# Performance work log

Hardware: AMD Instinct MI355X
Metric: run time of the kernel (lower is better)

Reference implementation:

```python
import jax, jax.numpy as jnp
import numpy as np

# dims: batch, seq, d_model, heads, n_buckets, n_hashes, d_ff
B, S, D, H, NB, R, DFF = 2, 4096, 1024, 16, 64, 4, 4096
DH = D // H          # head dim
C = S // NB          # attention chunk length after bucket sort
NCH = S // C         # number of chunks


def layernorm(x, g, b):
    m = x.mean(-1, keepdims=True)
    v = ((x - m) ** 2).mean(-1, keepdims=True)
    return (x - m) / jnp.sqrt(v + 1e-5) * g + b


def lsh_attention(x, Wqk, Wv, Wo, rot):
    Bx, Sx, _ = x.shape
    # shared QK projection (Reformer-style), separate V
    qk = (x @ Wqk).reshape(Bx, Sx, H, DH).transpose(0, 2, 1, 3)  # [B,H,S,dh]
    v = (x @ Wv).reshape(Bx, Sx, H, DH).transpose(0, 2, 1, 3)
    # random-rotation LSH: rot [dh, R, NB//2]
    rotated = jnp.einsum('bhsd,drk->rbhsk', qk, rot)
    buckets = jnp.argmax(jnp.concatenate([rotated, -rotated], -1), -1)  # [R,B,H,S]
    scale = DH ** -0.5
    pos = jnp.arange(Sx)

    def one_round(b_r):  # b_r: [B,H,S] bucket ids for one hash round
        order = jnp.argsort(b_r * Sx + pos, axis=-1)   # stable sort by bucket
        inv = jnp.argsort(order, axis=-1)
        sqk = jnp.take_along_axis(qk, order[..., None], 2)
        sv = jnp.take_along_axis(v, order[..., None], 2)
        sb = jnp.take_along_axis(b_r, order, -1)
        q_c = sqk.reshape(Bx, H, NCH, C, DH)
        # keys are L2-normalized shared qk
        k_c = (sqk / (jnp.linalg.norm(sqk, axis=-1, keepdims=True) + 1e-6)).reshape(Bx, H, NCH, C, DH)
        v_c = sv.reshape(Bx, H, NCH, C, DH)
        ext = lambda t: jnp.concatenate([t, jnp.roll(t, 1, axis=2)], axis=3)  # look back 1 chunk
        k_e, v_e = ext(k_c), ext(v_c)
        b_c = sb.reshape(Bx, H, NCH, C)
        b_e = jnp.concatenate([b_c, jnp.roll(b_c, 1, axis=2)], 3)
        p_c = order.reshape(Bx, H, NCH, C)
        p_e = jnp.concatenate([p_c, jnp.roll(p_c, 1, axis=2)], 3)
        s = jnp.einsum('bhnqd,bhnkd->bhnqk', q_c, k_e) * scale  # [B,H,nch,C,2C]
        s = jnp.where(b_c[..., :, None] == b_e[..., None, :], s, -1e9)   # only same bucket
        s = jnp.where(p_c[..., :, None] == p_e[..., None, :], -1e5, s)   # discourage self
        l = jax.scipy.special.logsumexp(s, -1)
        o = jnp.einsum('bhnqk,bhnkd->bhnqd', jax.nn.softmax(s, -1), v_e)
        o = o.reshape(Bx, H, Sx, DH)
        l = l.reshape(Bx, H, Sx)
        return jnp.take_along_axis(o, inv[..., None], 2), jnp.take_along_axis(l, inv, -1)

    o_all, l_all = jax.vmap(one_round)(buckets)        # [R,B,H,S,dh], [R,B,H,S]
    w = jax.nn.softmax(l_all, axis=0)[..., None]       # weight rounds by logsumexp
    out = (o_all * w).sum(0).transpose(0, 2, 1, 3).reshape(Bx, Sx, D)
    return out @ Wo


def feedforward(x, W1, b1, W2, b2):
    # chunked FF in the original only tiles the sequence dim; math is identical
    return jax.nn.relu(x @ W1 + b1) @ W2 + b2


def setup_inputs() -> dict:
    key = jax.random.key(0)
    ks = jax.random.split(key, 10)
    n = jax.random.normal
    return {
        'x1': n(ks[0], (B, S, D), jnp.float32),
        'x2': n(ks[1], (B, S, D), jnp.float32),
        'Wqk': n(ks[2], (D, D), jnp.float32) * (D ** -0.5),
        'Wv': n(ks[3], (D, D), jnp.float32) * (D ** -0.5),
        'Wo': n(ks[4], (D, D), jnp.float32) * (D ** -0.5),
        'ln1_g': jnp.ones(D, jnp.float32), 'ln1_b': jnp.zeros(D, jnp.float32),
        'W1': n(ks[5], (D, DFF), jnp.float32) * (D ** -0.5), 'bf1': jnp.zeros(DFF, jnp.float32),
        'W2': n(ks[6], (DFF, D), jnp.float32) * (DFF ** -0.5), 'bf2': jnp.zeros(D, jnp.float32),
        'ln2_g': jnp.ones(D, jnp.float32), 'ln2_b': jnp.zeros(D, jnp.float32),
        'rot': n(ks[7], (DH, R, NB // 2), jnp.float32),
    }


def reference(x1, x2, Wqk, Wv, Wo, ln1_g, ln1_b, W1, bf1, W2, bf2, ln2_g, ln2_b, rot):
    # reversible block: y1 = x1 + Attn(LN(x2)); y2 = x2 + FF(LN(y1))
    y1 = x1 + lsh_attention(layernorm(x2, ln1_g, ln1_b), Wqk, Wv, Wo, rot)
    y2 = x2 + feedforward(layernorm(y1, ln2_g, ln2_b), W1, bf1, W2, bf2)
    return (y1, y2)
```

## Files before the change

kernel.cpp:

```cpp
#include <hip/hip_runtime.h>
#include <hip/hip_bf16.h>
#include <math.h>

constexpr int CB   = 2;
constexpr int CS   = 4096;
constexpr int CD   = 1024;
constexpr int CH   = 16;
constexpr int CDH  = 64;
constexpr int CR   = 4;
constexpr int CC   = 64;
constexpr int CNCH = 64;
constexpr int CDFF = 4096;
constexpr int CBS  = CB * CS;
constexpr int CBHS = CB * CH * CS;

typedef __attribute__((ext_vector_type(8))) short short8;
typedef __attribute__((ext_vector_type(4))) short short4v;
typedef __attribute__((ext_vector_type(4))) float f32x4;

__device__ inline unsigned short f2bf(float f) {
    union { float f; unsigned int u; } a; a.f = f;
    unsigned int u = a.u;
    unsigned int r = (u + 0x7fffu + ((u >> 16) & 1u)) >> 16;
    return (unsigned short)r;
}
__device__ inline float bf2f(unsigned short h) {
    union { float f; unsigned int u; } a; a.u = ((unsigned int)h) << 16; return a.f;
}

#define AS3 __attribute__((address_space(3)))
#define AS1 __attribute__((address_space(1)))
__device__ inline void gload16(const unsigned short* g, unsigned short* l) {
    __builtin_amdgcn_global_load_lds((const AS1 unsigned int*)g,
                                     (AS3 unsigned int*)l, 16, 0, 0);
}

__device__ inline short8 ld_short8_u(const unsigned short* p) {
    short4v a = *(const short4v*)p;
    short4v b = *(const short4v*)(p + 4);
    short8 r;
    r[0] = a[0]; r[1] = a[1]; r[2] = a[2]; r[3] = a[3];
    r[4] = b[0]; r[5] = b[1]; r[6] = b[2]; r[7] = b[3];
    return r;
}
__device__ inline short8 pack8(float4 a, float4 b) {
    short8 r;
    r[0] = (short)f2bf(a.x); r[1] = (short)f2bf(a.y);
    r[2] = (short)f2bf(a.z); r[3] = (short)f2bf(a.w);
    r[4] = (short)f2bf(b.x); r[5] = (short)f2bf(b.y);
    r[6] = (short)f2bf(b.z); r[7] = (short)f2bf(b.w);
    return r;
}

__global__ __launch_bounds__(256) void ln_kernel(const float* __restrict__ x,
        const float* __restrict__ g, const float* __restrict__ bta,
        unsigned short* __restrict__ out16, unsigned short* __restrict__ out16lo) {
    int row = blockIdx.x;
    int t = threadIdx.x;
    const float* xr = x + (size_t)row * CD;
    float4 v = *(const float4*)(xr + t * 4);
    float s  = v.x + v.y + v.z + v.w;
    float ss = v.x * v.x + v.y * v.y + v.z * v.z + v.w * v.w;
    #pragma unroll
    for (int off = 1; off < 64; off <<= 1) {
        s  += __shfl_xor(s, off);
        ss += __shfl_xor(ss, off);
    }
    __shared__ float ws_[4], wss_[4];
    int wid = t >> 6;
    if ((t & 63) == 0) { ws_[wid] = s; wss_[wid] = ss; }
    __syncthreads();
    s  = ws_[0] + ws_[1] + ws_[2] + ws_[3];
    ss = wss_[0] + wss_[1] + wss_[2] + wss_[3];
    float mean = s * (1.0f / CD);
    float var  = ss * (1.0f / CD) - mean * mean;
    float rstd = rsqrtf(var + 1e-5f);
    float4 gv = *(const float4*)(g + t * 4);
    float4 bv = *(const float4*)(bta + t * 4);
    float4 o;
    o.x = (v.x - mean) * rstd * gv.x + bv.x;
    o.y = (v.y - mean) * rstd * gv.y + bv.y;
    o.z = (v.z - mean) * rstd * gv.z + bv.z;
    o.w = (v.w - mean) * rstd * gv.w + bv.w;
    ushort4 h; h.x = f2bf(o.x); h.y = f2bf(o.y); h.z = f2bf(o.z); h.w = f2bf(o.w);
    *(ushort4*)(out16 + (size_t)row * CD + t * 4) = h;
    if (out16lo) {
        ushort4 lo;
        lo.x = f2bf(o.x - bf2f(h.x)); lo.y = f2bf(o.y - bf2f(h.y));
        lo.z = f2bf(o.z - bf2f(h.z)); lo.w = f2bf(o.w - bf2f(h.w));
        *(ushort4*)(out16lo + (size_t)row * CD + t * 4) = lo;
    }
}

__global__ __launch_bounds__(256) void wtrans_kernel(const float* __restrict__ W,
        unsigned short* __restrict__ WT, unsigned short* __restrict__ WTlo,
        int K, int N) {
    __shared__ float tile[64][65];
    int n0 = blockIdx.x * 64, k0 = blockIdx.y * 64;
    int tid = threadIdx.x;
    int r = tid >> 4, c4 = tid & 15;
    #pragma unroll
    for (int it = 0; it < 4; ++it) {
        int row = r + it * 16;
        float4 v = *(const float4*)(W + (size_t)(k0 + row) * N + n0 + c4 * 4);
        tile[row][c4 * 4 + 0] = v.x; tile[row][c4 * 4 + 1] = v.y;
        tile[row][c4 * 4 + 2] = v.z; tile[row][c4 * 4 + 3] = v.w;
    }
    __syncthreads();
    #pragma unroll
    for (int it = 0; it < 4; ++it) {
        int nrow = r + it * 16;
        float f0 = tile[c4 * 4 + 0][nrow], f1 = tile[c4 * 4 + 1][nrow];
        float f2 = tile[c4 * 4 + 2][nrow], f3 = tile[c4 * 4 + 3][nrow];
        ushort4 h;
        h.x = f2bf(f0); h.y = f2bf(f1); h.z = f2bf(f2); h.w = f2bf(f3);
        *(ushort4*)(WT + (size_t)(n0 + nrow) * K + k0 + c4 * 4) = h;
        if (WTlo) {
            ushort4 lo;
            lo.x = f2bf(f0 - bf2f(h.x)); lo.y = f2bf(f1 - bf2f(h.y));
            lo.z = f2bf(f2 - bf2f(h.z)); lo.w = f2bf(f3 - bf2f(h.w));
            *(ushort4*)(WTlo + (size_t)(n0 + nrow) * K + k0 + c4 * 4) = lo;
        }
    }
}

template<int EPI>
__global__ __launch_bounds__(256) void gemm_bf16(const unsigned short* __restrict__ A,
        const unsigned short* __restrict__ BT, const float* __restrict__ bias,
        const float* __restrict__ res, void* __restrict__ outp,
        int M, int N, int K) {
    __shared__ __align__(16) unsigned short As[128 * 32];
    __shared__ __align__(16) unsigned short Bs[128 * 32];
    int tid = threadIdx.x;
    int w = tid >> 6, l = tid & 63;
    int m0 = blockIdx.y * 128, n0 = blockIdx.x * 128;
    int wm = (w >> 1) * 64, wn = (w & 1) * 64;

    const unsigned short* gA[2]; const unsigned short* gB[2];
    unsigned short* ldsA[2]; unsigned short* ldsB[2];
    int gchunk = (l & 3) ^ ((l >> 3) & 3);
    #pragma unroll
    for (int s = 0; s < 2; ++s) {
        int j = w * 2 + s;
        int R = j * 16 + (l >> 2);
        gA[s] = A + (size_t)(m0 + R) * K + gchunk * 8;
        gB[s] = BT + (size_t)(n0 + R) * K + gchunk * 8;
        ldsA[s] = As + j * 512;
        ldsB[s] = Bs + j * 512;
    }
    int p = (l >> 4) ^ (((l & 15) >> 1) & 3);
    int aoff = (wm + (l & 15)) * 32 + p * 8;
    int boff = (wn + (l & 15)) * 32 + p * 8;

    f32x4 acc[4][4];
    #pragma unroll
    for (int i = 0; i < 4; i++)
        #pragma unroll
        for (int j = 0; j < 4; j++) acc[i][j] = (f32x4)(0.f);

    for (int k0 = 0; k0 < K; k0 += 32) {
        gload16(gA[0] + k0, ldsA[0]);
        gload16(gA[1] + k0, ldsA[1]);
        gload16(gB[0] + k0, ldsB[0]);
        gload16(gB[1] + k0, ldsB[1]);
        __syncthreads();
        short8 af[4], bf[4];
        #pragma unroll
        for (int im = 0; im < 4; ++im) af[im] = *(const short8*)(As + aoff + im * 512);
        #pragma unroll
        for (int in = 0; in < 4; ++in) bf[in] = *(const short8*)(Bs + boff + in * 512);
        #pragma unroll
        for (int im = 0; im < 4; ++im)
            #pragma unroll
            for (int in = 0; in < 4; ++in)
                acc[im][in] = __builtin_amdgcn_mfma_f32_16x16x32_bf16(
                    af[im], bf[in], acc[im][in], 0, 0, 0);
        __syncthreads();
    }

    float bv[4];
    if (EPI == 1 || EPI == 2) {
        #pragma unroll
        for (int in = 0; in < 4; ++in) bv[in] = bias[n0 + wn + in * 16 + (l & 15)];
    }
    #pragma unroll
    for (int im = 0; im < 4; ++im) {
        #pragma unroll
        for (int in = 0; in < 4; ++in) {
            int n = n0 + wn + in * 16 + (l & 15);
            #pragma unroll
            for (int r = 0; r < 4; ++r) {
                int m = m0 + wm + im * 16 + (l >> 4) * 4 + r;
                float v = acc[im][in][r];
                if (EPI == 1) {
                    v = fmaxf(v + bv[in], 0.f);
                    ((unsigned short*)outp)[(size_t)m * N + n] = f2bf(v);
                } else {
                    if (EPI == 2) v += bv[in] + res[(size_t)m * N + n];
                    if (EPI == 3) v += res[(size_t)m * N + n];
                    ((float*)outp)[(size_t)m * N + n] = v;
                }
            }
        }
    }
}

__global__ __launch_bounds__(256) void gemm_bf16split(
        const unsigned short* __restrict__ Ah, const unsigned short* __restrict__ Al,
        const unsigned short* __restrict__ BTh, const unsigned short* __restrict__ BTl,
        float* __restrict__ outp, int M, int N, int K) {
    __shared__ __align__(16) unsigned short Ash[128 * 32];
    __shared__ __align__(16) unsigned short Asl[128 * 32];
    __shared__ __align__(16) unsigned short Bsh[128 * 32];
    __shared__ __align__(16) unsigned short Bsl[128 * 32];
    int tid = threadIdx.x;
    int w = tid >> 6, l = tid & 63;
    int m0 = blockIdx.y * 128, n0 = blockIdx.x * 128;
    int wm = (w >> 1) * 64, wn = (w & 1) * 64;

    size_t goff[2];
    unsigned short* ldsAh[2]; unsigned short* ldsAl[2];
    unsigned short* ldsBh[2]; unsigned short* ldsBl[2];
    size_t goffB[2];
    int gchunk = (l & 3) ^ ((l >> 3) & 3);
    #pragma unroll
    for (int s = 0; s < 2; ++s) {
        int j = w * 2 + s;
        int R = j * 16 + (l >> 2);
        goff[s]  = (size_t)(m0 + R) * K + gchunk * 8;
        goffB[s] = (size_t)(n0 + R) * K + gchunk * 8;
        ldsAh[s] = Ash + j * 512; ldsAl[s] = Asl + j * 512;
        ldsBh[s] = Bsh + j * 512; ldsBl[s] = Bsl + j * 512;
    }
    int p = (l >> 4) ^ (((l & 15) >> 1) & 3);
    int aoff = (wm + (l & 15)) * 32 + p * 8;
    int boff = (wn + (l & 15)) * 32 + p * 8;

    f32x4 acc[4][4];
    #pragma unroll
    for (int i = 0; i < 4; i++)
        #pragma unroll
        for (int j = 0; j < 4; j++) acc[i][j] = (f32x4)(0.f);

    for (int k0 = 0; k0 < K; k0 += 32) {
        #pragma unroll
        for (int s = 0; s < 2; ++s) {
            gload16(Ah  + goff[s]  + k0, ldsAh[s]);
            gload16(Al  + goff[s]  + k0, ldsAl[s]);
            gload16(BTh + goffB[s] + k0, ldsBh[s]);
            gload16(BTl + goffB[s] + k0, ldsBl[s]);
        }
        __syncthreads();
        short8 afh[4], afl[4], bfh[4], bfl[4];
        #pragma unroll
        for (int im = 0; im < 4; ++im) {
            afh[im] = *(const short8*)(Ash + aoff + im * 512);
            afl[im] = *(const short8*)(Asl + aoff + im * 512);
        }
        #pragma unroll
        for (int in = 0; in < 4; ++in) {
            bfh[in] = *(const short8*)(Bsh + boff + in * 512);
            bfl[in] = *(const short8*)(Bsl + boff + in * 512);
        }
        #pragma unroll
        for (int im = 0; im < 4; ++im)
            #pragma unroll
            for (int in = 0; in < 4; ++in) {
                acc[im][in] = __builtin_amdgcn_mfma_f32_16x16x32_bf16(
                    afh[im], bfh[in], acc[im][in], 0, 0, 0);
                acc[im][in] = __builtin_amdgcn_mfma_f32_16x16x32_bf16(
                    afl[im], bfh[in], acc[im][in], 0, 0, 0);
                acc[im][in] = __builtin_amdgcn_mfma_f32_16x16x32_bf16(
                    afh[im], bfl[in], acc[im][in], 0, 0, 0);
            }
        __syncthreads();
    }

    #pragma unroll
    for (int im = 0; im < 4; ++im)
        #pragma unroll
        for (int in = 0; in < 4; ++in) {
            int n = n0 + wn + in * 16 + (l & 15);
            #pragma unroll
            for (int r = 0; r < 4; ++r) {
                int m = m0 + wm + im * 16 + (l >> 4) * 4 + r;
                outp[(size_t)m * N + n] = acc[im][in][r];
            }
        }
}

template<int EPI>
__global__ __launch_bounds__(256) void gemm_f32(const float* __restrict__ A,
        const float* __restrict__ W, float* __restrict__ out,
        int M, int N, int K) {
    __shared__ __align__(16) float As[16][132];
    __shared__ __align__(16) float Bs[16][132];
    int tid = threadIdx.x;
    int n0 = blockIdx.x * 128;
    int m0 = blockIdx.y * 128;
    int ty = tid >> 4, tx = tid & 15;
    float acc[8][8];
    #pragma unroll
    for (int i = 0; i < 8; i++)
        #pragma unroll
        for (int j = 0; j < 8; j++) acc[i][j] = 0.f;

    for (int k0 = 0; k0 < K; k0 += 16) {
        #pragma unroll
        for (int it = 0; it < 2; ++it) {
            int f4 = tid + it * 256;
            int row = f4 >> 2, c4 = f4 & 3;
            float4 av = *(const float4*)(A + (size_t)(m0 + row) * K + k0 + c4 * 4);
            As[c4 * 4 + 0][row] = av.x;
            As[c4 * 4 + 1][row] = av.y;
            As[c4 * 4 + 2][row] = av.z;
            As[c4 * 4 + 3][row] = av.w;
        }
        #pragma unroll
        for (int it = 0; it < 2; ++it) {
            int f4 = tid + it * 256;
            int kr = f4 >> 5, c4 = f4 & 31;
            *(float4*)(&Bs[kr][c4 * 4]) =
                *(const float4*)(W + (size_t)(k0 + kr) * N + n0 + c4 * 4);
        }
        __syncthreads();
        #pragma unroll
        for (int kk = 0; kk < 16; ++kk) {
            float4 a0 = *(const float4*)(&As[kk][ty * 8]);
            float4 a1 = *(const float4*)(&As[kk][ty * 8 + 4]);
            float4 b0 = *(const float4*)(&Bs[kk][tx * 8]);
            float4 b1 = *(const float4*)(&Bs[kk][tx * 8 + 4]);
            float am[8] = {a0.x, a0.y, a0.z, a0.w, a1.x, a1.y, a1.z, a1.w};
            float bn[8] = {b0.x, b0.y, b0.z, b0.w, b1.x, b1.y, b1.z, b1.w};
            #pragma unroll
            for (int i = 0; i < 8; i++)
                #pragma unroll
                for (int j = 0; j < 8; j++)
                    acc[i][j] = fmaf(am[i], bn[j], acc[i][j]);
        }
        __syncthreads();
    }

    if (EPI == 4) {
        int* ibuck = (int*)out;
        int q = tx & 3, r = tx >> 2;
        #pragma unroll
        for (int i = 0; i < 8; i++) {
            int m = m0 + ty * 8 + i;
            float bestP = -3.4e38f, bestN = -3.4e38f;
            int biP = 0, biN = 0;
            #pragma unroll
            for (int j = 0; j < 8; j++) {
                float v = acc[i][j];
                if ( v > bestP) { bestP =  v; biP = q * 8 + j; }
                if (-v > bestN) { bestN = -v; biN = q * 8 + j; }
            }
            #pragma unroll
            for (int off = 1; off < 4; off <<= 1) {
                float oP = __shfl_xor(bestP, off); int oiP = __shfl_xor(biP, off);
                float oN = __shfl_xor(bestN, off); int oiN = __shfl_xor(biN, off);
                if (oP > bestP || (oP == bestP && oiP < biP)) { bestP = oP; biP = oiP; }
                if (oN > bestN || (oN == bestN && oiN < biN)) { bestN = oN; biN = oiN; }
            }
            if (q == 0) {
                int bi = (bestP >= bestN) ? biP : (biN + 32);
                int hh = m & 15, ss2 = (m >> 4) & (CS - 1), bb2 = m >> 16;
                ibuck[((size_t)((r * CB + bb2) * CH + hh)) * CS + ss2] = bi;
            }
        }
        return;
    }

    #pragma unroll
    for (int i = 0; i < 8; i++) {
        int m = m0 + ty * 8 + i;
        #pragma unroll
        for (int j4 = 0; j4 < 2; j4++) {
            int n = n0 + tx * 8 + j4 * 4;
            float4 v;
            v.x = acc[i][j4 * 4 + 0]; v.y = acc[i][j4 * 4 + 1];
            v.z = acc[i][j4 * 4 + 2]; v.w = acc[i][j4 * 4 + 3];
            *(float4*)(out + (size_t)m * N + n) = v;
        }
    }
}

__global__ __launch_bounds__(64) void sort_kernel(const int* __restrict__ buckets,
                                                  int* __restrict__ sorted_pos) {
    int g = blockIdx.x;
    const int* bk = buckets + (size_t)g * CS;
    __shared__ int hist[64][65];
    __shared__ int bstart[64];
    int t = threadIdx.x;
    #pragma unroll
    for (int i = 0; i < 64; i++) hist[t][i] = 0;
    __syncthreads();
    int base = t * 64;
    for (int i = 0; i < 64; i++) { int b = bk[base + i]; hist[t][b]++; }
    __syncthreads();
    int run = 0;
    for (int tt = 0; tt < 64; tt++) {
        int c = hist[tt][t];
        hist[tt][t] = run;
        run += c;
    }
    int x = run;
    #pragma unroll
    for (int off = 1; off < 64; off <<= 1) {
        int y = __shfl_up(x, off);
        if (t >= off) x += y;
    }
    bstart[t] = x - run;
    __syncthreads();
    for (int i = 0; i < 64; i++) {
        int b = bk[base + i];
        int rank = bstart[b] + hist[t][b];
        hist[t][b]++;
        sorted_pos[(size_t)g * CS + rank] = base + i;
    }
}

__global__ __launch_bounds__(256) void attn_kernel(const float* __restrict__ qkbuf,
        const float* __restrict__ vbuf, const int* __restrict__ buckets,
        const int* __restrict__ sorted, unsigned short* __restrict__ o_all,
        float* __restrict__ l_all) {
    int n  = blockIdx.x;
    int r  = blockIdx.y;
    int bh = blockIdx.z;
    int b = bh >> 4, h = bh & 15;
    int rbh = (r * CB + b) * CH + h;
    int tid = threadIdx.x;
    int w = tid >> 6, l = tid & 63;
    int l4 = l & 15, qd = l >> 4;

    __shared__ int pk[128];
    __shared__ int bkk[128];
    __shared__ __align__(16) unsigned short Ks[128 * 72];
    __shared__ __align__(16) unsigned short Ps[64 * 132];
    __shared__ __align__(16) unsigned short VsT[64 * 132];

    int prev = (n + CNCH - 1) & (CNCH - 1);
    if (tid < 128) {
        int i = tid & 63;
        int ch = (tid < 64) ? n : prev;
        int p = sorted[(size_t)rbh * CS + ch * CC + i];
        pk[tid] = p;
        bkk[tid] = buckets[(size_t)rbh * CS + p];
    }
    __syncthreads();

    const float* qbase = qkbuf + (size_t)b * CS * CD + h * 64;
    const float* vbase = vbuf  + (size_t)b * CS * CD + h * 64;

    #pragma unroll
    for (int it = 0; it < 8; ++it) {
        int f4 = tid + it * 256;
        int kk = f4 >> 4, d4 = f4 & 15;
        float4 v = *(const float4*)(qbase + (size_t)pk[kk] * CD + d4 * 4);
        float ss = v.x * v.x + v.y * v.y + v.z * v.z + v.w * v.w;
        ss += __shfl_xor(ss, 1); ss += __shfl_xor(ss, 2);
        ss += __shfl_xor(ss, 4); ss += __shfl_xor(ss, 8);
        float rn = 1.f / (sqrtf(ss) + 1e-6f);
        ushort4 hv;
        hv.x = f2bf(v.x * rn); hv.y = f2bf(v.y * rn);
        hv.z = f2bf(v.z * rn); hv.w = f2bf(v.w * rn);
        *(ushort4*)&Ks[kk * 72 + d4 * 4] = hv;
    }
    #pragma unroll
    for (int it = 0; it < 16; ++it) {
        int kkp = w * 16 + it;
        int r0 = pk[2 * kkp], r1 = pk[2 * kkp + 1];
        float v0 = vbase[(size_t)r0 * CD + l];
        float v1 = vbase[(size_t)r1 * CD + l];
        unsigned int pck = (unsigned int)f2bf(v0) | ((unsigned int)f2bf(v1) << 16);
        *(unsigned int*)&VsT[l * 132 + 2 * kkp] = pck;
    }
    int mstrip = w * 16;
    const float* qptr = qbase + (size_t)pk[mstrip + l4] * CD + qd * 8;
    float4 qa0 = *(const float4*)(qptr);
    float4 qa1 = *(const float4*)(qptr + 4);
    float4 qb0 = *(const float4*)(qptr + 32);
    float4 qb1 = *(const float4*)(qptr + 36);
    short8 afA = pack8(qa0, qa1);
    short8 afB = pack8(qb0, qb1);
    __syncthreads();

    f32x4 sa[8];
    #pragma unroll
    for (int t = 0; t < 8; ++t) sa[t] = (f32x4)(0.f);
    #pragma unroll
    for (int t = 0; t < 8; ++t) {
        const unsigned short* kb = &Ks[(t * 16 + l4) * 72 + qd * 8];
        short8 b0 = *(const short8*)(kb);
        short8 b1 = *(const short8*)(kb + 32);
        sa[t] = __builtin_amdgcn_mfma_f32_16x16x32_bf16(afA, b0, sa[t], 0, 0, 0);
        sa[t] = __builtin_amdgcn_mfma_f32_16x16x32_bf16(afB, b1, sa[t], 0, 0, 0);
    }

    int rowb[4], rowp[4];
    #pragma unroll
    for (int rr = 0; rr < 4; ++rr) {
        int m = mstrip + 4 * qd + rr;
        rowb[rr] = bkk[m]; rowp[rr] = pk[m];
    }
    float mx[4] = {-3.4e38f, -3.4e38f, -3.4e38f, -3.4e38f};
    #pragma unroll
    for (int t = 0; t < 8; ++t) {
        int cb = bkk[t * 16 + l4], cp = pk[t * 16 + l4];
        #pragma unroll
        for (int rr = 0; rr < 4; ++rr) {
            float v = sa[t][rr] * 0.125f;
            if (rowb[rr] != cb) v = -1e9f;
            if (rowp[rr] == cp) v = -1e5f;
            sa[t][rr] = v;
            mx[rr] = fmaxf(mx[rr], v);
        }
    }
    #pragma unroll
    for (int rr = 0; rr < 4; ++rr) {
        mx[rr] = fmaxf(mx[rr], __shfl_xor(mx[rr], 1));
        mx[rr] = fmaxf(mx[rr], __shfl_xor(mx[rr], 2));
        mx[rr] = fmaxf(mx[rr], __shfl_xor(mx[rr], 4));
        mx[rr] = fmaxf(mx[rr], __shfl_xor(mx[rr], 8));
    }
    float sum[4] = {0.f, 0.f, 0.f, 0.f};
    #pragma unroll
    for (int t = 0; t < 8; ++t)
        #pragma unroll
        for (int rr = 0; rr < 4; ++rr) {
            float e = expf(sa[t][rr] - mx[rr]);
            sa[t][rr] = e;
            sum[rr] += e;
        }
    #pragma unroll
    for (int rr = 0; rr < 4; ++rr) {
        sum[rr] += __shfl_xor(sum[rr], 1);
        sum[rr] += __shfl_xor(sum[rr], 2);
        sum[rr] += __shfl_xor(sum[rr], 4);
        sum[rr] += __shfl_xor(sum[rr], 8);
    }
    if (l4 == 0) {
        #pragma unroll
        for (int rr = 0; rr < 4; ++rr)
            l_all[(size_t)rbh * CS + rowp[rr]] = mx[rr] + logf(sum[rr]);
    }

    float rs[4];
    #pragma unroll
    for (int rr = 0; rr < 4; ++rr) rs[rr] = 1.f / sum[rr];
    #pragma unroll
    for (int t = 0; t < 8; ++t)
        #pragma unroll
        for (int rr = 0; rr < 4; ++rr)
            Ps[(mstrip + 4 * qd + rr) * 132 + t * 16 + l4] = f2bf(sa[t][rr] * rs[rr]);

    f32x4 oa[4];
    #pragma unroll
    for (int nt = 0; nt < 4; ++nt) oa[nt] = (f32x4)(0.f);
    #pragma unroll
    for (int ks = 0; ks < 4; ++ks) {
        short8 ap = ld_short8_u(&Ps[(mstrip + l4) * 132 + ks * 32 + qd * 8]);
        #pragma unroll
        for (int nt = 0; nt < 4; ++nt) {
            short8 bv = ld_short8_u(&VsT[(nt * 16 + l4) * 132 + ks * 32 + qd * 8]);
            oa[nt] = __builtin_amdgcn_mfma_f32_16x16x32_bf16(ap, bv, oa[nt], 0, 0, 0);
        }
    }
    #pragma unroll
    for (int nt = 0; nt < 4; ++nt)
        #pragma unroll
        for (int rr = 0; rr < 4; ++rr)
            o_all[((size_t)rbh * CS + rowp[rr]) * CDH + nt * 16 + l4] = f2bf(oa[nt][rr]);
}

__global__ __launch_bounds__(256) void combine_kernel(const unsigned short* __restrict__ o_all,
        const float* __restrict__ l_all, unsigned short* __restrict__ attnout16) {
    int idx = blockIdx.x * 256 + threadIdx.x;
    int d = idx & 63, bhs = idx >> 6;
    int s2 = bhs & (CS - 1), bh = bhs >> 12, h = bh & 15, b = bh >> 4;
    float lr[4];
    #pragma unroll
    for (int r = 0; r < CR; r++) lr[r] = l_all[(size_t)r * CBHS + bhs];
    float m = fmaxf(fmaxf(lr[0], lr[1]), fmaxf(lr[2], lr[3]));
    float w[4], sum = 0.f;
    #pragma unroll
    for (int r = 0; r < CR; r++) { w[r] = expf(lr[r] - m); sum += w[r]; }
    float acc = 0.f;
    #pragma unroll
    for (int r = 0; r < CR; r++)
        acc += w[r] * bf2f(o_all[((size_t)r * CBHS + bhs) * CDH + d]);
    acc /= sum;
    attnout16[((size_t)(b * CS + s2)) * CD + h * 64 + d] = f2bf(acc);
}

extern "C" void kernel_launch(void* const* d_in, const int* in_sizes, int n_in,
                              void* d_out, int out_size, void* d_ws, size_t ws_size,
                              hipStream_t stream) {
    const float* x1   = (const float*)d_in[0];
    const float* x2   = (const float*)d_in[1];
    const float* Wqk  = (const float*)d_in[2];
    const float* Wv   = (const float*)d_in[3];
    const float* Wo   = (const float*)d_in[4];
    const float* ln1g = (const float*)d_in[5];
    const float* ln1b = (const float*)d_in[6];
    const float* W1   = (const float*)d_in[7];
    const float* bf1  = (const float*)d_in[8];
    const float* W2   = (const float*)d_in[9];
    const float* bf2  = (const float*)d_in[10];
    const float* ln2g = (const float*)d_in[11];
    const float* ln2b = (const float*)d_in[12];
    const float* rot  = (const float*)d_in[13];

    unsigned short* bufA16   = (unsigned short*)d_ws;
    unsigned short* bufA16lo = bufA16 + (size_t)CBS * CD;
    float* bufB = (float*)(bufA16lo + (size_t)CBS * CD);
    float* bufC = bufB + (size_t)CBS * CD;
    unsigned short* o_all = (unsigned short*)(bufC + (size_t)CBS * CD);
    float* l_all  = (float*)(o_all + (size_t)CR * CBHS * CDH);
    int* buckets  = (int*)(l_all + (size_t)CR * CBHS);
    int* sorted   = buckets + (size_t)CR * CBHS;
    unsigned short* WvT   = (unsigned short*)(sorted + (size_t)CR * CBHS);
    unsigned short* WoT   = WvT + (size_t)CD * CD;
    unsigned short* W1T   = WoT + (size_t)CD * CD;
    unsigned short* W2T   = W1T + (size_t)CD * CDFF;
    unsigned short* WqkTh = W2T + (size_t)CD * CDFF;
    unsigned short* WqkTl = WqkTh + (size_t)CD * CD;
    unsigned short* ffh16 = (unsigned short*)bufB;
    unsigned short* attnout16 = bufA16;
    unsigned short* lnY16 = bufA16;
    float* y1 = (float*)d_out;
    float* y2 = y1 + (size_t)CBS * CD;

    wtrans_kernel<<<dim3(CD / 64, CD / 64), 256, 0, stream>>>(Wqk, WqkTh, WqkTl, CD, CD);
    wtrans_kernel<<<dim3(CD / 64, CD / 64), 256, 0, stream>>>(Wv, WvT, nullptr, CD, CD);
    wtrans_kernel<<<dim3(CD / 64, CD / 64), 256, 0, stream>>>(Wo, WoT, nullptr, CD, CD);
    wtrans_kernel<<<dim3(CDFF / 64, CD / 64), 256, 0, stream>>>(W1, W1T, nullptr, CD, CDFF);
    wtrans_kernel<<<dim3(CD / 64, CDFF / 64), 256, 0, stream>>>(W2, W2T, nullptr, CDFF, CD);
    ln_kernel<<<CBS, 256, 0, stream>>>(x2, ln1g, ln1b, bufA16, bufA16lo);
    gemm_bf16split<<<dim3(CD / 128, CBS / 128), 256, 0, stream>>>(
        bufA16, bufA16lo, WqkTh, WqkTl, bufB, CBS, CD, CD);
    gemm_bf16<0><<<dim3(CD / 128, CBS / 128), 256, 0, stream>>>(bufA16, WvT, nullptr, nullptr, bufC, CBS, CD, CD);
    gemm_f32<4><<<dim3(1, CBHS / 128), 256, 0, stream>>>(bufB, rot, (float*)buckets, CBHS, 128, 64);
    sort_kernel<<<CR * CB * CH, 64, 0, stream>>>(buckets, sorted);
    attn_kernel<<<dim3(CNCH, CR, CB * CH), 256, 0, stream>>>(bufB, bufC, buckets, sorted, o_all, l_all);
    combine_kernel<<<(CBHS * CDH) / 256, 256, 0, stream>>>(o_all, l_all, attnout16);
    gemm_bf16<3><<<dim3(CD / 128, CBS / 128), 256, 0, stream>>>(attnout16, WoT, nullptr, x1, y1, CBS, CD, CD);
    ln_kernel<<<CBS, 256, 0, stream>>>(y1, ln2g, ln2b, lnY16, nullptr);
    gemm_bf16<1><<<dim3(CDFF / 128, CBS / 128), 256, 0, stream>>>(lnY16, W1T, bf1, nullptr, ffh16, CBS, CDFF, CD);
    gemm_bf16<2><<<dim3(CD / 128, CBS / 128), 256, 0, stream>>>(ffh16, W2T, bf2, x2, y2, CBS, CD, CDFF);
}
```

Measured before the change: 714.6 us.

## Template GEMM tile height, swizzle workgroups, emit bf16 QK/V, use fast math intrinsics

The GEMM kernels take a template row-tile height, and the smaller N=1024 GEMMs switch to 64-row tiles so more workgroups fill the GPU. Workgroup IDs are remapped across groups of eight. The QK and V projections now also write bf16 copies, so the attention kernel reads half the bytes and skips its own conversions. Float-to-bf16 conversion uses the hardware cast, and exp, log and division use fast intrinsics. The trade-off is lower per-tile reuse, an extra bf16 store in the QK GEMM, and slightly different rounding and approximation.

```diff
diff --git a/kernel.cpp b/kernel.cpp
--- a/kernel.cpp
+++ b/kernel.cpp
@@ -19,10 +19,12 @@
 typedef __attribute__((ext_vector_type(4))) float f32x4;
 
 __device__ inline unsigned short f2bf(float f) {
-    union { float f; unsigned int u; } a; a.f = f;
-    unsigned int u = a.u;
-    unsigned int r = (u + 0x7fffu + ((u >> 16) & 1u)) >> 16;
-    return (unsigned short)r;
+    __bf16 h = (__bf16)f;
+    union { __bf16 h; unsigned short u; } c; c.h = h;
+    return c.u;
+}
+__device__ inline unsigned int cvt2(float a, float b) {
+    return (unsigned int)f2bf(a) | ((unsigned int)f2bf(b) << 16);
 }
 __device__ inline float bf2f(unsigned short h) {
     union { float f; unsigned int u; } a; a.u = ((unsigned int)h) << 16; return a.f;
@@ -41,14 +43,6 @@
     short8 r;
     r[0] = a[0]; r[1] = a[1]; r[2] = a[2]; r[3] = a[3];
     r[4] = b[0]; r[5] = b[1]; r[6] = b[2]; r[7] = b[3];
-    return r;
-}
-__device__ inline short8 pack8(float4 a, float4 b) {
-    short8 r;
-    r[0] = (short)f2bf(a.x); r[1] = (short)f2bf(a.y);
-    r[2] = (short)f2bf(a.z); r[3] = (short)f2bf(a.w);
-    r[4] = (short)f2bf(b.x); r[5] = (short)f2bf(b.y);
-    r[6] = (short)f2bf(b.z); r[7] = (short)f2bf(b.w);
     return r;
 }
 
@@ -124,53 +118,63 @@
     }
 }
 
-template<int EPI>
+template<int EPI, int BM>
 __global__ __launch_bounds__(256) void gemm_bf16(const unsigned short* __restrict__ A,
         const unsigned short* __restrict__ BT, const float* __restrict__ bias,
         const float* __restrict__ res, void* __restrict__ outp,
         int M, int N, int K) {
-    __shared__ __align__(16) unsigned short As[128 * 32];
+    constexpr int SA  = BM / 64;
+    constexpr int MI2 = BM / 32;
+    __shared__ __align__(16) unsigned short As[BM * 32];
     __shared__ __align__(16) unsigned short Bs[128 * 32];
     int tid = threadIdx.x;
     int w = tid >> 6, l = tid & 63;
-    int m0 = blockIdx.y * 128, n0 = blockIdx.x * 128;
-    int wm = (w >> 1) * 64, wn = (w & 1) * 64;
-
-    const unsigned short* gA[2]; const unsigned short* gB[2];
-    unsigned short* ldsA[2]; unsigned short* ldsB[2];
+    int nwg = gridDim.x * gridDim.y;
+    int lid = blockIdx.y * gridDim.x + blockIdx.x;
+    if (!(nwg & 7)) lid = (lid & 7) * (nwg >> 3) + (lid >> 3);
+    int m0 = (lid / gridDim.x) * BM, n0 = (lid % gridDim.x) * 128;
+    int wm = (w >> 1) * (BM / 2), wn = (w & 1) * 64;
+
+    const unsigned short* gA[SA]; const unsigned short* gB[2];
+    unsigned short* ldsA[SA]; unsigned short* ldsB[2];
     int gchunk = (l & 3) ^ ((l >> 3) & 3);
+    #pragma unroll
+    for (int s = 0; s < SA; ++s) {
+        int j = w * SA + s;
+        int R = j * 16 + (l >> 2);
+        gA[s] = A + (size_t)(m0 + R) * K + gchunk * 8;
+        ldsA[s] = As + j * 512;
+    }
     #pragma unroll
     for (int s = 0; s < 2; ++s) {
         int j = w * 2 + s;
         int R = j * 16 + (l >> 2);
-        gA[s] = A + (size_t)(m0 + R) * K + gchunk * 8;
         gB[s] = BT + (size_t)(n0 + R) * K + gchunk * 8;
-        ldsA[s] = As + j * 512;
         ldsB[s] = Bs + j * 512;
     }
     int p = (l >> 4) ^ (((l & 15) >> 1) & 3);
     int aoff = (wm + (l & 15)) * 32 + p * 8;
     int boff = (wn + (l & 15)) * 32 + p * 8;
 
-    f32x4 acc[4][4];
-    #pragma unroll
-    for (int i = 0; i < 4; i++)
+    f32x4 acc[MI2][4];
+    #pragma unroll
+    for (int i = 0; i < MI2; i++)
         #pragma unroll
         for (int j = 0; j < 4; j++) acc[i][j] = (f32x4)(0.f);
 
     for (int k0 = 0; k0 < K; k0 += 32) {
-        gload16(gA[0] + k0, ldsA[0]);
-        gload16(gA[1] + k0, ldsA[1]);
+        #pragma unroll
+        for (int s = 0; s < SA; ++s) gload16(gA[s] + k0, ldsA[s]);
         gload16(gB[0] + k0, ldsB[0]);
         gload16(gB[1] + k0, ldsB[1]);
         __syncthreads();
-        short8 af[4], bf[4];
-        #pragma unroll
-        for (int im = 0; im < 4; ++im) af[im] = *(const short8*)(As + aoff + im * 512);
+        short8 af[MI2], bf[4];
+        #pragma unroll
+        for (int im = 0; im < MI2; ++im) af[im] = *(const short8*)(As + aoff + im * 512);
         #pragma unroll
         for (int in = 0; in < 4; ++in) bf[in] = *(const short8*)(Bs + boff + in * 512);
         #pragma unroll
-        for (int im = 0; im < 4; ++im)
+        for (int im = 0; im < MI2; ++im)
             #pragma unroll
             for (int in = 0; in < 4; ++in)
                 acc[im][in] = __builtin_amdgcn_mfma_f32_16x16x32_bf16(
@@ -184,7 +188,7 @@
         for (int in = 0; in < 4; ++in) bv[in] = bias[n0 + wn + in * 16 + (l & 15)];
     }
     #pragma unroll
-    for (int im = 0; im < 4; ++im) {
+    for (int im = 0; im < MI2; ++im) {
         #pragma unroll
         for (int in = 0; in < 4; ++in) {
             int n = n0 + wn + in * 16 + (l & 15);
@@ -195,6 +199,8 @@
                 if (EPI == 1) {
                     v = fmaxf(v + bv[in], 0.f);
                     ((unsigned short*)outp)[(size_t)m * N + n] = f2bf(v);
+                } else if (EPI == 5) {
+                    ((unsigned short*)outp)[(size_t)m * N + n] = f2bf(v);
                 } else {
                     if (EPI == 2) v += bv[in] + res[(size_t)m * N + n];
                     if (EPI == 3) v += res[(size_t)m * N + n];
@@ -205,55 +211,69 @@
     }
 }
 
+template<int BM>
 __global__ __launch_bounds__(256) void gemm_bf16split(
         const unsigned short* __restrict__ Ah, const unsigned short* __restrict__ Al,
         const unsigned short* __restrict__ BTh, const unsigned short* __restrict__ BTl,
-        float* __restrict__ outp, int M, int N, int K) {
-    __shared__ __align__(16) unsigned short Ash[128 * 32];
-    __shared__ __align__(16) unsigned short Asl[128 * 32];
+        float* __restrict__ outp, unsigned short* __restrict__ out16,
+        int M, int N, int K) {
+    constexpr int SA  = BM / 64;
+    constexpr int MI2 = BM / 32;
+    __shared__ __align__(16) unsigned short Ash[BM * 32];
+    __shared__ __align__(16) unsigned short Asl[BM * 32];
     __shared__ __align__(16) unsigned short Bsh[128 * 32];
     __shared__ __align__(16) unsigned short Bsl[128 * 32];
     int tid = threadIdx.x;
     int w = tid >> 6, l = tid & 63;
-    int m0 = blockIdx.y * 128, n0 = blockIdx.x * 128;
-    int wm = (w >> 1) * 64, wn = (w & 1) * 64;
-
-    size_t goff[2];
-    unsigned short* ldsAh[2]; unsigned short* ldsAl[2];
+    int nwg = gridDim.x * gridDim.y;
+    int lid = blockIdx.y * gridDim.x + blockIdx.x;
+    if (!(nwg & 7)) lid = (lid & 7) * (nwg >> 3) + (lid >> 3);
+    int m0 = (lid / gridDim.x) * BM, n0 = (lid % gridDim.x) * 128;
+    int wm = (w >> 1) * (BM / 2), wn = (w & 1) * 64;
+
+    size_t goffA[SA]; size_t goffB[2];
+    unsigned short* ldsAh[SA]; unsigned short* ldsAl[SA];
     unsigned short* ldsBh[2]; unsigned short* ldsBl[2];
-    size_t goffB[2];
     int gchunk = (l & 3) ^ ((l >> 3) & 3);
+    #pragma unroll
+    for (int s = 0; s < SA; ++s) {
+        int j = w * SA + s;
+        int R = j * 16 + (l >> 2);
+        goffA[s] = (size_t)(m0 + R) * K + gchunk * 8;
+        ldsAh[s] = Ash + j * 512; ldsAl[s] = Asl + j * 512;
+    }
     #pragma unroll
     for (int s = 0; s < 2; ++s) {
         int j = w * 2 + s;
         int R = j * 16 + (l >> 2);
-        goff[s]  = (size_t)(m0 + R) * K + gchunk * 8;
         goffB[s] = (size_t)(n0 + R) * K + gchunk * 8;
-        ldsAh[s] = Ash + j * 512; ldsAl[s] = Asl + j * 512;
         ldsBh[s] = Bsh + j * 512; ldsBl[s] = Bsl + j * 512;
     }
     int p = (l >> 4) ^ (((l & 15) >> 1) & 3);
     int aoff = (wm + (l & 15)) * 32 + p * 8;
     int boff = (wn + (l & 15)) * 32 + p * 8;
 
-    f32x4 acc[4][4];
-    #pragma unroll
-    for (int i = 0; i < 4; i++)
+    f32x4 acc[MI2][4];
+    #pragma unroll
+    for (int i = 0; i < MI2; i++)
         #pragma unroll
         for (int j = 0; j < 4; j++) acc[i][j] = (f32x4)(0.f);
 
     for (int k0 = 0; k0 < K; k0 += 32) {
         #pragma unroll
+        for (int s = 0; s < SA; ++s) {
+            gload16(Ah + goffA[s] + k0, ldsAh[s]);
+            gload16(Al + goffA[s] + k0, ldsAl[s]);
+        }
+        #pragma unroll
         for (int s = 0; s < 2; ++s) {
-            gload16(Ah  + goff[s]  + k0, ldsAh[s]);
-            gload16(Al  + goff[s]  + k0, ldsAl[s]);
             gload16(BTh + goffB[s] + k0, ldsBh[s]);
             gload16(BTl + goffB[s] + k0, ldsBl[s]);
         }
         __syncthreads();
-        short8 afh[4], afl[4], bfh[4], bfl[4];
-        #pragma unroll
-        for (int im = 0; im < 4; ++im) {
+        short8 afh[MI2], afl[MI2], bfh[4], bfl[4];
+        #pragma unroll
+        for (int im = 0; im < MI2; ++im) {
             afh[im] = *(const short8*)(Ash + aoff + im * 512);
             afl[im] = *(const short8*)(Asl + aoff + im * 512);
         }
@@ -263,7 +283,7 @@
             bfl[in] = *(const short8*)(Bsl + boff + in * 512);
         }
         #pragma unroll
-        for (int im = 0; im < 4; ++im)
+        for (int im = 0; im < MI2; ++im)
             #pragma unroll
             for (int in = 0; in < 4; ++in) {
                 acc[im][in] = __builtin_amdgcn_mfma_f32_16x16x32_bf16(
@@ -277,14 +297,16 @@
     }
 
     #pragma unroll
-    for (int im = 0; im < 4; ++im)
+    for (int im = 0; im < MI2; ++im)
         #pragma unroll
         for (int in = 0; in < 4; ++in) {
             int n = n0 + wn + in * 16 + (l & 15);
             #pragma unroll
             for (int r = 0; r < 4; ++r) {
                 int m = m0 + wm + im * 16 + (l >> 4) * 4 + r;
-                outp[(size_t)m * N + n] = acc[im][in][r];
+                float v = acc[im][in][r];
+                outp[(size_t)m * N + n] = v;
+                out16[(size_t)m * N + n] = f2bf(v);
             }
         }
 }
@@ -420,8 +442,8 @@
     }
 }
 
-__global__ __launch_bounds__(256) void attn_kernel(const float* __restrict__ qkbuf,
-        const float* __restrict__ vbuf, const int* __restrict__ buckets,
+__global__ __launch_bounds__(256) void attn_kernel(const unsigned short* __restrict__ qk16,
+        const unsigned short* __restrict__ v16, const int* __restrict__ buckets,
         const int* __restrict__ sorted, unsigned short* __restrict__ o_all,
         float* __restrict__ l_all) {
     int n  = blockIdx.x;
@@ -449,40 +471,36 @@
     }
     __syncthreads();
 
-    const float* qbase = qkbuf + (size_t)b * CS * CD + h * 64;
-    const float* vbase = vbuf  + (size_t)b * CS * CD + h * 64;
+    const unsigned short* qbase = qk16 + (size_t)b * CS * CD + h * 64;
+    const unsigned short* vbase = v16  + (size_t)b * CS * CD + h * 64;
 
     #pragma unroll
     for (int it = 0; it < 8; ++it) {
         int f4 = tid + it * 256;
         int kk = f4 >> 4, d4 = f4 & 15;
-        float4 v = *(const float4*)(qbase + (size_t)pk[kk] * CD + d4 * 4);
-        float ss = v.x * v.x + v.y * v.y + v.z * v.z + v.w * v.w;
+        ushort4 hv = *(const ushort4*)(qbase + (size_t)pk[kk] * CD + d4 * 4);
+        float x0 = bf2f(hv.x), x1 = bf2f(hv.y), x2 = bf2f(hv.z), x3 = bf2f(hv.w);
+        float ss = x0 * x0 + x1 * x1 + x2 * x2 + x3 * x3;
         ss += __shfl_xor(ss, 1); ss += __shfl_xor(ss, 2);
         ss += __shfl_xor(ss, 4); ss += __shfl_xor(ss, 8);
-        float rn = 1.f / (sqrtf(ss) + 1e-6f);
-        ushort4 hv;
-        hv.x = f2bf(v.x * rn); hv.y = f2bf(v.y * rn);
-        hv.z = f2bf(v.z * rn); hv.w = f2bf(v.w * rn);
-        *(ushort4*)&Ks[kk * 72 + d4 * 4] = hv;
+        float rn = __builtin_amdgcn_rcpf(sqrtf(ss) + 1e-6f);
+        uint2 kp;
+        kp.x = cvt2(x0 * rn, x1 * rn);
+        kp.y = cvt2(x2 * rn, x3 * rn);
+        *(uint2*)&Ks[kk * 72 + d4 * 4] = kp;
     }
     #pragma unroll
     for (int it = 0; it < 16; ++it) {
         int kkp = w * 16 + it;
         int r0 = pk[2 * kkp], r1 = pk[2 * kkp + 1];
-        float v0 = vbase[(size_t)r0 * CD + l];
-        float v1 = vbase[(size_t)r1 * CD + l];
-        unsigned int pck = (unsigned int)f2bf(v0) | ((unsigned int)f2bf(v1) << 16);
-        *(unsigned int*)&VsT[l * 132 + 2 * kkp] = pck;
+        unsigned int u0 = vbase[(size_t)r0 * CD + l];
+        unsigned int u1 = vbase[(size_t)r1 * CD + l];
+        *(unsigned int*)&VsT[l * 132 + 2 * kkp] = u0 | (u1 << 16);
     }
     int mstrip = w * 16;
-    const float* qptr = qbase + (size_t)pk[mstrip + l4] * CD + qd * 8;
-    float4 qa0 = *(const float4*)(qptr);
-    float4 qa1 = *(const float4*)(qptr + 4);
-    float4 qb0 = *(const float4*)(qptr + 32);
-    float4 qb1 = *(const float4*)(qptr + 36);
-    short8 afA = pack8(qa0, qa1);
-    short8 afB = pack8(qb0, qb1);
+    const unsigned short* qptr = qbase + (size_t)pk[mstrip + l4] * CD + qd * 8;
+    short8 afA = *(const short8*)(qptr);
+    short8 afB = *(const short8*)(qptr + 32);
     __syncthreads();
 
     f32x4 sa[8];
@@ -528,7 +546,7 @@
     for (int t = 0; t < 8; ++t)
         #pragma unroll
         for (int rr = 0; rr < 4; ++rr) {
-            float e = expf(sa[t][rr] - mx[rr]);
+            float e = __expf(sa[t][rr] - mx[rr]);
             sa[t][rr] = e;
             sum[rr] += e;
         }
@@ -542,17 +560,22 @@
     if (l4 == 0) {
         #pragma unroll
         for (int rr = 0; rr < 4; ++rr)
-            l_all[(size_t)rbh * CS + rowp[rr]] = mx[rr] + logf(sum[rr]);
+            l_all[(size_t)rbh * CS + rowp[rr]] = mx[rr] + __logf(sum[rr]);
     }
 
     float rs[4];
     #pragma unroll
-    for (int rr = 0; rr < 4; ++rr) rs[rr] = 1.f / sum[rr];
-    #pragma unroll
-    for (int t = 0; t < 8; ++t)
-        #pragma unroll
-        for (int rr = 0; rr < 4; ++rr)
-            Ps[(mstrip + 4 * qd + rr) * 132 + t * 16 + l4] = f2bf(sa[t][rr] * rs[rr]);
+    for (int rr = 0; rr < 4; ++rr) rs[rr] = __builtin_amdgcn_rcpf(sum[rr]);
+    #pragma unroll
+    for (int t = 0; t < 8; ++t) {
+        unsigned int a01 = cvt2(sa[t][0] * rs[0], sa[t][1] * rs[1]);
+        unsigned int a23 = cvt2(sa[t][2] * rs[2], sa[t][3] * rs[3]);
+        int base = (mstrip + 4 * qd) * 132 + t * 16 + l4;
+        Ps[base]       = (unsigned short)(a01 & 0xffffu);
+        Ps[base + 132] = (unsigned short)(a01 >> 16);
+        Ps[base + 264] = (unsigned short)(a23 & 0xffffu);
+        Ps[base + 396] = (unsigned short)(a23 >> 16);
+    }
 
     f32x4 oa[4];
     #pragma unroll
@@ -566,11 +589,16 @@
             oa[nt] = __builtin_amdgcn_mfma_f32_16x16x32_bf16(ap, bv, oa[nt], 0, 0, 0);
         }
     }
-    #pragma unroll
-    for (int nt = 0; nt < 4; ++nt)
-        #pragma unroll
-        for (int rr = 0; rr < 4; ++rr)
-            o_all[((size_t)rbh * CS + rowp[rr]) * CDH + nt * 16 + l4] = f2bf(oa[nt][rr]);
+    size_t ob = (size_t)rbh * CS;
+    #pragma unroll
+    for (int nt = 0; nt < 4; ++nt) {
+        unsigned int a01 = cvt2(oa[nt][0], oa[nt][1]);
+        unsigned int a23 = cvt2(oa[nt][2], oa[nt][3]);
+        o_all[(ob + rowp[0]) * CDH + nt * 16 + l4] = (unsigned short)(a01 & 0xffffu);
+        o_all[(ob + rowp[1]) * CDH + nt * 16 + l4] = (unsigned short)(a01 >> 16);
+        o_all[(ob + rowp[2]) * CDH + nt * 16 + l4] = (unsigned short)(a23 & 0xffffu);
+        o_all[(ob + rowp[3]) * CDH + nt * 16 + l4] = (unsigned short)(a23 >> 16);
+    }
 }
 
 __global__ __launch_bounds__(256) void combine_kernel(const unsigned short* __restrict__ o_all,
@@ -584,12 +612,12 @@
     float m = fmaxf(fmaxf(lr[0], lr[1]), fmaxf(lr[2], lr[3]));
     float w[4], sum = 0.f;
     #pragma unroll
-    for (int r = 0; r < CR; r++) { w[r] = expf(lr[r] - m); sum += w[r]; }
+    for (int r = 0; r < CR; r++) { w[r] = __expf(lr[r] - m); sum += w[r]; }
     float acc = 0.f;
     #pragma unroll
     for (int r = 0; r < CR; r++)
         acc += w[r] * bf2f(o_all[((size_t)r * CBHS + bhs) * CDH + d]);
-    acc /= sum;
+    acc *= __builtin_amdgcn_rcpf(sum);
     attnout16[((size_t)(b * CS + s2)) * CD + h * 64 + d] = f2bf(acc);
 }
 
@@ -615,6 +643,8 @@
     unsigned short* bufA16lo = bufA16 + (size_t)CBS * CD;
     float* bufB = (float*)(bufA16lo + (size_t)CBS * CD);
     float* bufC = bufB + (size_t)CBS * CD;
+    unsigned short* v16  = (unsigned short*)bufC;
+    unsigned short* qk16 = v16 + (size_t)CBS * CD;
     unsigned short* o_all = (unsigned short*)(bufC + (size_t)CBS * CD);
     float* l_all  = (float*)(o_all + (size_t)CR * CBHS * CDH);
     int* buckets  = (int*)(l_all + (size_t)CR * CBHS);
@@ -637,15 +667,19 @@
     wtrans_kernel<<<dim3(CDFF / 64, CD / 64), 256, 0, stream>>>(W1, W1T, nullptr, CD, CDFF);
     wtrans_kernel<<<dim3(CD / 64, CDFF / 64), 256, 0, stream>>>(W2, W2T, nullptr, CDFF, CD);
     ln_kernel<<<CBS, 256, 0, stream>>>(x2, ln1g, ln1b, bufA16, bufA16lo);
-    gemm_bf16split<<<dim3(CD / 128, CBS / 128), 256, 0, stream>>>(
-        bufA16, bufA16lo, WqkTh, WqkTl, bufB, CBS, CD, CD);
-    gemm_bf16<0><<<dim3(CD / 128, CBS / 128), 256, 0, stream>>>(bufA16, WvT, nullptr, nullptr, bufC, CBS, CD, CD);
+    gemm_bf16split<64><<<dim3(CD / 128, CBS / 64), 256, 0, stream>>>(
+        bufA16, bufA16lo, WqkTh, WqkTl, bufB, qk16, CBS, CD, CD);
+    gemm_bf16<5, 64><<<dim3(CD / 128, CBS / 64), 256, 0, stream>>>(
+        bufA16, WvT, nullptr, nullptr, v16, CBS, CD, CD);
     gemm_f32<4><<<dim3(1, CBHS / 128), 256, 0, stream>>>(bufB, rot, (float*)buckets, CBHS, 128, 64);
     sort_kernel<<<CR * CB * CH, 64, 0, stream>>>(buckets, sorted);
-    attn_kernel<<<dim3(CNCH, CR, CB * CH), 256, 0, stream>>>(bufB, bufC, buckets, sorted, o_all, l_all);
+    attn_kernel<<<dim3(CNCH, CR, CB * CH), 256, 0, stream>>>(qk16, v16, buckets, sorted, o_all, l_all);
     combine_kernel<<<(CBHS * CDH) / 256, 256, 0, stream>>>(o_all, l_all, attnout16);
-    gemm_bf16<3><<<dim3(CD / 128, CBS / 128), 256, 0, stream>>>(attnout16, WoT, nullptr, x1, y1, CBS, CD, CD);
+    gemm_bf16<3, 64><<<dim3(CD / 128, CBS / 64), 256, 0, stream>>>(
+        attnout16, WoT, nullptr, x1, y1, CBS, CD, CD);
     ln_kernel<<<CBS, 256, 0, stream>>>(y1, ln2g, ln2b, lnY16, nullptr);
-    gemm_bf16<1><<<dim3(CDFF / 128, CBS / 128), 256, 0, stream>>>(lnY16, W1T, bf1, nullptr, ffh16, CBS, CDFF, CD);
-    gemm_bf16<2><<<dim3(CD / 128, CBS / 128), 256, 0, stream>>>(ffh16, W2T, bf2, x2, y2, CBS, CD, CDFF);
-}
+    gemm_bf16<1, 128><<<dim3(CDFF / 128, CBS / 128), 256, 0, stream>>>(
+        lnY16, W1T, bf1, nullptr, ffh16, CBS, CDFF, CD);
+    gemm_bf16<2, 64><<<dim3(CD / 128, CBS / 64), 256, 0, stream>>>(
+        ffh16, W2T, bf2, x2, y2, CBS, CD, CDFF);
+}
```

Result: faster. 655.5 us (-8.3%).
